# Optimization experiments

Measured on AMD Instinct MI355X. Metric: run time of the kernel, lower is better.

The kernel has to match this reference:

```python
import jax, jax.numpy as jnp
import numpy as np

COORD_DIM = 4
HIDDEN = 256
N_HIDDEN_LAYERS = 4  # num_layers - 1 hidden->hidden layers after the first
MIN_OMEGA = 10.0
MAX_OMEGA = 100.0
MEDIAN_OMEGA = (MIN_OMEGA + MAX_OMEGA) / 2.0
N = 524288


def _uniform(key, shape, bound):
    return jax.random.uniform(key, shape, jnp.float32, -bound, bound)


def setup_inputs() -> dict:
    key = jax.random.key(0)
    ks = jax.random.split(key, 16)
    coords = jax.random.normal(ks[0], (N, COORD_DIM), jnp.float32)
    # omega predictor: Linear(4, 64) -> ReLU -> Linear(64, 1) -> Sigmoid
    ow1 = _uniform(ks[1], (COORD_DIM, HIDDEN // 4), 1.0 / np.sqrt(COORD_DIM))
    ob1 = _uniform(ks[2], (HIDDEN // 4,), 1.0 / np.sqrt(COORD_DIM))
    ow2 = _uniform(ks[3], (HIDDEN // 4, 1), 1.0 / np.sqrt(HIDDEN // 4))
    ob2 = _uniform(ks[4], (1,), 1.0 / np.sqrt(HIDDEN // 4))
    # SIREN first layer: uniform(-1/in_features, 1/in_features)
    w0 = _uniform(ks[5], (COORD_DIM, HIDDEN), 1.0 / COORD_DIM)
    b0 = _uniform(ks[6], (HIDDEN,), 1.0 / np.sqrt(COORD_DIM))
    # SIREN hidden layers: uniform(-sqrt(6/in)/omega0, ...), stacked [4, 256, 256]
    hb = np.sqrt(6.0 / HIDDEN) / MEDIAN_OMEGA
    wh = _uniform(ks[7], (N_HIDDEN_LAYERS, HIDDEN, HIDDEN), hb)
    bh = _uniform(ks[8], (N_HIDDEN_LAYERS, HIDDEN), 1.0 / np.sqrt(HIDDEN))
    wf = _uniform(ks[9], (HIDDEN, 1), hb)
    bf = _uniform(ks[10], (1,), 1.0 / np.sqrt(HIDDEN))
    return {"coords": coords, "ow1": ow1, "ob1": ob1, "ow2": ow2, "ob2": ob2,
            "w0": w0, "b0": b0, "wh": wh, "bh": bh, "wf": wf, "bf": bf}


def reference(coords, ow1, ob1, ow2, ob2, w0, b0, wh, bh, wf, bf):
    # adaptive omega per coordinate: [N, 1]
    h = jax.nn.relu(coords @ ow1 + ob1)
    omega = MIN_OMEGA + (MAX_OMEGA - MIN_OMEGA) * jax.nn.sigmoid(h @ ow2 + ob2)
    # SIREN stack: x = sin(omega * (x @ W + b))
    x = jnp.sin(omega * (coords @ w0 + b0))
    for i in range(N_HIDDEN_LAYERS):
        x = jnp.sin(omega * (x @ wh[i] + bh[i]))
    return x @ wf + bf  # [N, 1]
```

## Files before the change

kernel.cpp:

```cpp
#include <hip/hip_runtime.h>
#include <hip/hip_bf16.h>

typedef _Float16 f16;
typedef f16 f16x4 __attribute__((ext_vector_type(4)));
typedef f16 f16x8 __attribute__((ext_vector_type(8)));
typedef float f32x4 __attribute__((ext_vector_type(4)));
typedef float f32x16 __attribute__((ext_vector_type(16)));

#define MT 256
#define LDST 260
#define INV2PI 0.15915494309189535f

__global__ __launch_bounds__(64)
void prep_wt(const float* __restrict__ wh, f16* __restrict__ wt) {
    const int b = blockIdx.x;
    const int layer = b >> 7, wcblk = (b >> 4) & 7, kblk = b & 15;
    const int lane = threadIdx.x;
    const int l31 = lane & 31, lh = lane >> 5;
    const float* src = wh + layer * 65536 + (kblk * 16 + lh * 8) * 256 + wcblk * 32 + l31;
    f16x8 v;
#pragma unroll
    for (int j = 0; j < 8; j++) v[j] = (f16)src[j * 256];
    *(f16x8*)(wt + b * 512 + lane * 8) = v;
}

__device__ inline f16x8 lds_ld8(const f16* p) {
    f16x4 lo = *(const f16x4*)p;
    f16x4 hi = *(const f16x4*)(p + 4);
    return __builtin_shufflevector(lo, hi, 0, 1, 2, 3, 4, 5, 6, 7);
}

__global__ __launch_bounds__(512, 2)
void siren_fused(const float* __restrict__ coords,
                 const float* __restrict__ ow1, const float* __restrict__ ob1,
                 const float* __restrict__ ow2, const float* __restrict__ ob2,
                 const float* __restrict__ w0, const float* __restrict__ b0,
                 const f16* __restrict__ wt,
                 const float* __restrict__ bh,
                 const float* __restrict__ wf,
                 const float* __restrict__ bf,
                 float* __restrict__ out) {
    __shared__ __align__(16) f16 Xs[MT * LDST];
    __shared__ float om_rev[MT];
    __shared__ __align__(16) float crd[MT * 4];
    __shared__ __align__(16) float bh_s[256];
    __shared__ __align__(16) float wf_s[256];

    const int t = threadIdx.x;
    const long base_pt = (long)blockIdx.x * MT;

    if (t < 256) {
        ((f32x4*)crd)[t] = ((const f32x4*)(coords + base_pt * 4))[t];
        wf_s[t] = wf[t];
    }
    __syncthreads();

    if (t < 256) {
        const float c0 = crd[t * 4], c1 = crd[t * 4 + 1], c2 = crd[t * 4 + 2], c3 = crd[t * 4 + 3];
        float h[64];
#pragma unroll
        for (int j = 0; j < 64; j++) {
            float z = ob1[j] + c0 * ow1[j] + c1 * ow1[64 + j] + c2 * ow1[128 + j] + c3 * ow1[192 + j];
            h[j] = fmaxf(z, 0.f);
        }
        float z2 = ob2[0];
#pragma unroll
        for (int j = 0; j < 64; j++) z2 += h[j] * ow2[j];
        const float sig = 1.f / (1.f + __expf(-z2));
        om_rev[t] = (10.f + 90.f * sig) * INV2PI;
    }
    __syncthreads();

    {
        const int pt = t >> 1;
        const int ch = (t & 1) * 128;
        const float c0 = crd[pt * 4], c1 = crd[pt * 4 + 1], c2 = crd[pt * 4 + 2], c3 = crd[pt * 4 + 3];
        const float orv = om_rev[pt];
#pragma unroll 4
        for (int c = 0; c < 128; c += 4) {
            f32x4 wv0 = *(const f32x4*)(w0 + 0 * 256 + ch + c);
            f32x4 wv1 = *(const f32x4*)(w0 + 1 * 256 + ch + c);
            f32x4 wv2 = *(const f32x4*)(w0 + 2 * 256 + ch + c);
            f32x4 wv3 = *(const f32x4*)(w0 + 3 * 256 + ch + c);
            f32x4 bv  = *(const f32x4*)(b0 + ch + c);
            f16x4 r;
#pragma unroll
            for (int j = 0; j < 4; j++) {
                float z = bv[j] + c0 * wv0[j] + c1 * wv1[j] + c2 * wv2[j] + c3 * wv3[j];
                r[j] = (f16)__builtin_amdgcn_sinf(orv * z);
            }
            *(f16x4*)&Xs[pt * LDST + ch + c] = r;
        }
    }
    __syncthreads();

    const int lane = t & 63;
    const int wave = t >> 6;
    const int l31 = lane & 31;
    const int lh = lane >> 5;
    const int wc0 = (wave & 3) * 64;
    const int pr0 = (wave >> 2) * 128;

    for (int layer = 0; layer < 4; layer++) {
        if (t < 256) bh_s[t] = bh[layer * 256 + t];

        const f16* afrag = wt + ((layer * 8 + (wave & 3) * 2) * 16) * 512 + lane * 8;
        const f16* bptr = &Xs[(pr0 + l31) * LDST + lh * 8];

        f32x16 acc[2][4];
#pragma unroll
        for (int ct = 0; ct < 2; ct++)
#pragma unroll
            for (int rt = 0; rt < 4; rt++)
#pragma unroll
                for (int j = 0; j < 16; j++) acc[ct][rt][j] = 0.f;

#pragma unroll
        for (int kb = 0; kb < 16; kb++) {
            f16x8 av0 = *(const f16x8*)(afrag + kb * 512);
            f16x8 av1 = *(const f16x8*)(afrag + 8192 + kb * 512);
            f16x8 bv[4];
#pragma unroll
            for (int rt = 0; rt < 4; rt++) bv[rt] = lds_ld8(bptr + rt * 32 * LDST + kb * 16);
#pragma unroll
            for (int rt = 0; rt < 4; rt++) {
                acc[0][rt] = __builtin_amdgcn_mfma_f32_32x32x16_f16(av0, bv[rt], acc[0][rt], 0, 0, 0);
                acc[1][rt] = __builtin_amdgcn_mfma_f32_32x32x16_f16(av1, bv[rt], acc[1][rt], 0, 0, 0);
            }
        }
        __syncthreads();

        float orv[4];
#pragma unroll
        for (int rt = 0; rt < 4; rt++) orv[rt] = om_rev[pr0 + rt * 32 + l31];
#pragma unroll
        for (int ct = 0; ct < 2; ct++) {
#pragma unroll
            for (int g = 0; g < 4; g++) {
                const int wc = wc0 + ct * 32 + g * 8 + lh * 4;
                f32x4 bb = *(const f32x4*)&bh_s[wc];
#pragma unroll
                for (int rt = 0; rt < 4; rt++) {
                    const int prow = pr0 + rt * 32 + l31;
                    f16x4 r;
#pragma unroll
                    for (int j = 0; j < 4; j++) {
                        float z = acc[ct][rt][g * 4 + j] + bb[j];
                        r[j] = (f16)__builtin_amdgcn_sinf(orv[rt] * z);
                    }
                    *(f16x4*)&Xs[prow * LDST + wc] = r;
                }
            }
        }
        __syncthreads();
    }

    {
        const int pt = t >> 1;
        const int ch = (t & 1) * 128;
        const f16* xrow = &Xs[pt * LDST + ch];
        float s = 0.f;
#pragma unroll 8
        for (int c = 0; c < 128; c += 4) {
            f16x4 xv = *(const f16x4*)(xrow + c);
            f32x4 wv = *(const f32x4*)&wf_s[ch + c];
            s += (float)xv[0] * wv[0] + (float)xv[1] * wv[1]
               + (float)xv[2] * wv[2] + (float)xv[3] * wv[3];
        }
        s += __shfl_xor(s, 1, 64);
        if ((t & 1) == 0) out[base_pt + pt] = s + bf[0];
    }
}

extern "C" void kernel_launch(void* const* d_in, const int* in_sizes, int n_in,
                              void* d_out, int out_size, void* d_ws, size_t ws_size,
                              hipStream_t stream) {
    (void)in_sizes; (void)n_in; (void)out_size; (void)ws_size;
    const float* coords = (const float*)d_in[0];
    const float* ow1 = (const float*)d_in[1];
    const float* ob1 = (const float*)d_in[2];
    const float* ow2 = (const float*)d_in[3];
    const float* ob2 = (const float*)d_in[4];
    const float* w0  = (const float*)d_in[5];
    const float* b0  = (const float*)d_in[6];
    const float* wh  = (const float*)d_in[7];
    const float* bh  = (const float*)d_in[8];
    const float* wf  = (const float*)d_in[9];
    const float* bf  = (const float*)d_in[10];
    float* out = (float*)d_out;
    f16* wt = (f16*)d_ws;

    prep_wt<<<512, 64, 0, stream>>>(wh, wt);
    siren_fused<<<524288 / MT, 512, 0, stream>>>(coords, ow1, ob1, ow2, ob2,
                                                 w0, b0, wt, bh, wf, bf, out);
}
```

Measured before the change: 520.4 us.

## Halve tile to 128 points per block for higher occupancy and pack f16 conversions

```diff
diff --git a/kernel.cpp b/kernel.cpp
--- a/kernel.cpp
+++ b/kernel.cpp
@@ -4,10 +4,12 @@
 typedef _Float16 f16;
 typedef f16 f16x4 __attribute__((ext_vector_type(4)));
 typedef f16 f16x8 __attribute__((ext_vector_type(8)));
+typedef __fp16 h16x2 __attribute__((ext_vector_type(2)));
+typedef __fp16 h16x4 __attribute__((ext_vector_type(4)));
 typedef float f32x4 __attribute__((ext_vector_type(4)));
 typedef float f32x16 __attribute__((ext_vector_type(16)));
 
-#define MT 256
+#define MT 128
 #define LDST 260
 #define INV2PI 0.15915494309189535f
 
@@ -30,7 +32,14 @@
     return __builtin_shufflevector(lo, hi, 0, 1, 2, 3, 4, 5, 6, 7);
 }
 
-__global__ __launch_bounds__(512, 2)
+__device__ inline f16x4 pk4(float z0, float z1, float z2, float z3) {
+    h16x2 a = __builtin_amdgcn_cvt_pkrtz(z0, z1);
+    h16x2 b = __builtin_amdgcn_cvt_pkrtz(z2, z3);
+    h16x4 r = __builtin_shufflevector(a, b, 0, 1, 2, 3);
+    return __builtin_bit_cast(f16x4, r);
+}
+
+__global__ __launch_bounds__(512, 4)
 void siren_fused(const float* __restrict__ coords,
                  const float* __restrict__ ow1, const float* __restrict__ ob1,
                  const float* __restrict__ ow2, const float* __restrict__ ob2,
@@ -49,13 +58,11 @@
     const int t = threadIdx.x;
     const long base_pt = (long)blockIdx.x * MT;
 
-    if (t < 256) {
-        ((f32x4*)crd)[t] = ((const f32x4*)(coords + base_pt * 4))[t];
-        wf_s[t] = wf[t];
-    }
+    if (t < MT) ((f32x4*)crd)[t] = ((const f32x4*)(coords + base_pt * 4))[t];
+    if (t < 256) wf_s[t] = wf[t];
     __syncthreads();
 
-    if (t < 256) {
+    if (t < MT) {
         const float c0 = crd[t * 4], c1 = crd[t * 4 + 1], c2 = crd[t * 4 + 2], c3 = crd[t * 4 + 3];
         float h[64];
 #pragma unroll
@@ -72,24 +79,24 @@
     __syncthreads();
 
     {
-        const int pt = t >> 1;
-        const int ch = (t & 1) * 128;
+        const int pt = t >> 2;
+        const int ch = (t & 3) * 64;
         const float c0 = crd[pt * 4], c1 = crd[pt * 4 + 1], c2 = crd[pt * 4 + 2], c3 = crd[pt * 4 + 3];
         const float orv = om_rev[pt];
 #pragma unroll 4
-        for (int c = 0; c < 128; c += 4) {
+        for (int c = 0; c < 64; c += 4) {
             f32x4 wv0 = *(const f32x4*)(w0 + 0 * 256 + ch + c);
             f32x4 wv1 = *(const f32x4*)(w0 + 1 * 256 + ch + c);
             f32x4 wv2 = *(const f32x4*)(w0 + 2 * 256 + ch + c);
             f32x4 wv3 = *(const f32x4*)(w0 + 3 * 256 + ch + c);
             f32x4 bv  = *(const f32x4*)(b0 + ch + c);
-            f16x4 r;
+            float z[4];
 #pragma unroll
             for (int j = 0; j < 4; j++) {
-                float z = bv[j] + c0 * wv0[j] + c1 * wv1[j] + c2 * wv2[j] + c3 * wv3[j];
-                r[j] = (f16)__builtin_amdgcn_sinf(orv * z);
+                float zz = bv[j] + c0 * wv0[j] + c1 * wv1[j] + c2 * wv2[j] + c3 * wv3[j];
+                z[j] = __builtin_amdgcn_sinf(orv * zz);
             }
-            *(f16x4*)&Xs[pt * LDST + ch + c] = r;
+            *(f16x4*)&Xs[pt * LDST + ch + c] = pk4(z[0], z[1], z[2], z[3]);
         }
     }
     __syncthreads();
@@ -98,20 +105,21 @@
     const int wave = t >> 6;
     const int l31 = lane & 31;
     const int lh = lane >> 5;
-    const int wc0 = (wave & 3) * 64;
-    const int pr0 = (wave >> 2) * 128;
+    const int wcg = wave & 3;
+    const int pr0 = (wave >> 2) * 64;
+    const int wc0 = wcg * 64;
 
     for (int layer = 0; layer < 4; layer++) {
         if (t < 256) bh_s[t] = bh[layer * 256 + t];
 
-        const f16* afrag = wt + ((layer * 8 + (wave & 3) * 2) * 16) * 512 + lane * 8;
+        const f16* afrag = wt + ((layer * 8 + wcg * 2) * 16) * 512 + lane * 8;
         const f16* bptr = &Xs[(pr0 + l31) * LDST + lh * 8];
 
-        f32x16 acc[2][4];
+        f32x16 acc[2][2];
 #pragma unroll
         for (int ct = 0; ct < 2; ct++)
 #pragma unroll
-            for (int rt = 0; rt < 4; rt++)
+            for (int rt = 0; rt < 2; rt++)
 #pragma unroll
                 for (int j = 0; j < 16; j++) acc[ct][rt][j] = 0.f;
 
@@ -119,20 +127,20 @@
         for (int kb = 0; kb < 16; kb++) {
             f16x8 av0 = *(const f16x8*)(afrag + kb * 512);
             f16x8 av1 = *(const f16x8*)(afrag + 8192 + kb * 512);
-            f16x8 bv[4];
-#pragma unroll
-            for (int rt = 0; rt < 4; rt++) bv[rt] = lds_ld8(bptr + rt * 32 * LDST + kb * 16);
-#pragma unroll
-            for (int rt = 0; rt < 4; rt++) {
+            f16x8 bv[2];
+#pragma unroll
+            for (int rt = 0; rt < 2; rt++) bv[rt] = lds_ld8(bptr + rt * 32 * LDST + kb * 16);
+#pragma unroll
+            for (int rt = 0; rt < 2; rt++) {
                 acc[0][rt] = __builtin_amdgcn_mfma_f32_32x32x16_f16(av0, bv[rt], acc[0][rt], 0, 0, 0);
                 acc[1][rt] = __builtin_amdgcn_mfma_f32_32x32x16_f16(av1, bv[rt], acc[1][rt], 0, 0, 0);
             }
         }
         __syncthreads();
 
-        float orv[4];
-#pragma unroll
-        for (int rt = 0; rt < 4; rt++) orv[rt] = om_rev[pr0 + rt * 32 + l31];
+        float orv[2];
+#pragma unroll
+        for (int rt = 0; rt < 2; rt++) orv[rt] = om_rev[pr0 + rt * 32 + l31];
 #pragma unroll
         for (int ct = 0; ct < 2; ct++) {
 #pragma unroll
@@ -140,15 +148,13 @@
                 const int wc = wc0 + ct * 32 + g * 8 + lh * 4;
                 f32x4 bb = *(const f32x4*)&bh_s[wc];
 #pragma unroll
-                for (int rt = 0; rt < 4; rt++) {
+                for (int rt = 0; rt < 2; rt++) {
                     const int prow = pr0 + rt * 32 + l31;
-                    f16x4 r;
-#pragma unroll
-                    for (int j = 0; j < 4; j++) {
-                        float z = acc[ct][rt][g * 4 + j] + bb[j];
-                        r[j] = (f16)__builtin_amdgcn_sinf(orv[rt] * z);
-                    }
-                    *(f16x4*)&Xs[prow * LDST + wc] = r;
+                    float z[4];
+#pragma unroll
+                    for (int j = 0; j < 4; j++)
+                        z[j] = __builtin_amdgcn_sinf(orv[rt] * (acc[ct][rt][g * 4 + j] + bb[j]));
+                    *(f16x4*)&Xs[prow * LDST + wc] = pk4(z[0], z[1], z[2], z[3]);
                 }
             }
         }
@@ -156,19 +162,20 @@
     }
 
     {
-        const int pt = t >> 1;
-        const int ch = (t & 1) * 128;
+        const int pt = t >> 2;
+        const int ch = (t & 3) * 64;
         const f16* xrow = &Xs[pt * LDST + ch];
         float s = 0.f;
 #pragma unroll 8
-        for (int c = 0; c < 128; c += 4) {
+        for (int c = 0; c < 64; c += 4) {
             f16x4 xv = *(const f16x4*)(xrow + c);
             f32x4 wv = *(const f32x4*)&wf_s[ch + c];
             s += (float)xv[0] * wv[0] + (float)xv[1] * wv[1]
                + (float)xv[2] * wv[2] + (float)xv[3] * wv[3];
         }
         s += __shfl_xor(s, 1, 64);
-        if ((t & 1) == 0) out[base_pt + pt] = s + bf[0];
+        s += __shfl_xor(s, 2, 64);
+        if ((t & 3) == 0) out[base_pt + pt] = s + bf[0];
     }
 }
 
```

After: 619.0 us. 19.0% more time.
